# Kernel tuning notes

Measured on AMD Instinct MI355X. Metric: run time of the kernel, lower is better.

Reference implementation:

```python
import jax, jax.numpy as jnp
import numpy as np

N = 1048576   # samples
C = 64        # classes (Y unique targets)
S = 8         # subgroups


def setup_inputs() -> dict:
    key = jax.random.key(0)
    k1, k2, k3 = jax.random.split(key, 3)
    logits = jax.random.normal(k1, (N, C), dtype=jnp.float32)
    targets = jax.random.randint(k2, (N,), 0, C, dtype=jnp.int64)
    subgroup_inf = jax.random.randint(k3, (N,), 0, S, dtype=jnp.int64)
    return {"logits": logits, "targets": targets, "subgroup_inf": subgroup_inf}


def reference(logits, targets, subgroup_inf):
    # per-sample cross-entropy (loss_fn with reduction='none')
    logp = jax.nn.log_softmax(logits, axis=-1)                       # [N, C]
    per_sample = -jnp.take_along_axis(logp, targets[:, None], axis=-1)[:, 0]  # [N]

    # composite (target, subgroup) key -> group counts via one scatter-add
    key_ids = targets * S + subgroup_inf                              # [N]
    counts = jax.ops.segment_sum(jnp.ones_like(per_sample), key_ids,
                                 num_segments=C * S)                  # [C*S]
    # every sample's own group has count >= 1, so no div-by-zero
    weighted = per_sample / counts[key_ids]
    return jnp.sum(weighted)
```

## Files before the change

kernel.cpp:

```cpp
#include <hip/hip_runtime.h>


#define NKEYS 512
#define NSLICES 512
#define ABLOCK 512
typedef float v4f __attribute__((ext_vector_type(4)));

__device__ __forceinline__ float pick4(v4f v, int j) {
    float r = v.x;
    r = (j == 1) ? v.y : r;
    r = (j == 2) ? v.z : r;
    r = (j == 3) ? v.w : r;
    return r;
}

__device__ __forceinline__ float esum4(v4f v) {
    return __expf(v.x) + __expf(v.y) + __expf(v.z) + __expf(v.w);
}

__global__ __launch_bounds__(ABLOCK, 4)
void orl_hist_kernel(const float* __restrict__ logits,
                     const int* __restrict__ targets,
                     const int* __restrict__ subg,
                     float* __restrict__ psum,
                     unsigned int* __restrict__ pcnt,
                     int n) {
    __shared__ float        lsum[NKEYS];
    __shared__ unsigned int lcnt[NKEYS];
    for (int i = threadIdx.x; i < NKEYS; i += ABLOCK) { lsum[i] = 0.0f; lcnt[i] = 0u; }
    __syncthreads();

    const int lane = threadIdx.x & 63;
    const int q    = lane & 15;
    const int g    = lane >> 4;
    const int wave = (blockIdx.x << 3) | (threadIdx.x >> 6);
    const int nwaves = gridDim.x << 3;

    int base = wave * 16;
    for (; base + 16 <= n; base += nwaves * 16) {
        const int r0 = base + g * 4;
        const int4 t4 = *(const int4*)(targets + r0);
        const int4 u4 = *(const int4*)(subg + r0);
        const float* rowp = logits + (size_t)r0 * 64 + q * 4;
        const v4f v0 = __builtin_nontemporal_load((const v4f*)(rowp));
        const v4f v1 = __builtin_nontemporal_load((const v4f*)(rowp + 64));
        const v4f v2 = __builtin_nontemporal_load((const v4f*)(rowp + 128));
        const v4f v3 = __builtin_nontemporal_load((const v4f*)(rowp + 192));

        float s0 = esum4(v0), s1 = esum4(v1), s2 = esum4(v2), s3 = esum4(v3);
        #pragma unroll
        for (int m = 1; m < 16; m <<= 1) {
            s0 += __shfl_xor(s0, m, 16);
            s1 += __shfl_xor(s1, m, 16);
            s2 += __shfl_xor(s2, m, 16);
            s3 += __shfl_xor(s3, m, 16);
        }
        if ((t4.x >> 2) == q) {
            const float ps = __logf(s0) - pick4(v0, t4.x & 3);
            atomicAdd(&lsum[t4.x * 8 + u4.x], ps); atomicAdd(&lcnt[t4.x * 8 + u4.x], 1u);
        }
        if ((t4.y >> 2) == q) {
            const float ps = __logf(s1) - pick4(v1, t4.y & 3);
            atomicAdd(&lsum[t4.y * 8 + u4.y], ps); atomicAdd(&lcnt[t4.y * 8 + u4.y], 1u);
        }
        if ((t4.z >> 2) == q) {
            const float ps = __logf(s2) - pick4(v2, t4.z & 3);
            atomicAdd(&lsum[t4.z * 8 + u4.z], ps); atomicAdd(&lcnt[t4.z * 8 + u4.z], 1u);
        }
        if ((t4.w >> 2) == q) {
            const float ps = __logf(s3) - pick4(v3, t4.w & 3);
            atomicAdd(&lsum[t4.w * 8 + u4.w], ps); atomicAdd(&lcnt[t4.w * 8 + u4.w], 1u);
        }
    }
    for (int o = 0; o < 4; ++o) {
        const int r = base + g * 4 + o;
        if (r < n) {
            const v4f v = *((const v4f*)(logits + (size_t)r * 64) + q);
            const int t = targets[r];
            float s = esum4(v);
            #pragma unroll
            for (int m = 1; m < 16; m <<= 1) s += __shfl_xor(s, m, 16);
            if ((t >> 2) == q) {
                const float ps = __logf(s) - pick4(v, t & 3);
                const int key = t * 8 + subg[r];
                atomicAdd(&lsum[key], ps); atomicAdd(&lcnt[key], 1u);
            }
        }
    }

    __syncthreads();
    const size_t sbase = (size_t)blockIdx.x * NKEYS;
    for (int i = threadIdx.x; i < NKEYS; i += ABLOCK) {
        psum[sbase + i] = lsum[i];
        pcnt[sbase + i] = lcnt[i];
    }
}

__global__ __launch_bounds__(256)
void orl_reduce_kernel(const float* __restrict__ psum,
                       const unsigned int* __restrict__ pcnt,
                       float* __restrict__ out) {
    const int kk  = threadIdx.x & 7;
    const int sl  = threadIdx.x >> 3;
    const int key = (blockIdx.x << 3) | kk;
    float s = 0.0f; unsigned int c = 0u;
    #pragma unroll 4
    for (int b = sl; b < NSLICES; b += 32) {
        s += psum[(size_t)b * NKEYS + key];
        c += pcnt[(size_t)b * NKEYS + key];
    }
    #pragma unroll
    for (int m = 8; m < 64; m <<= 1) {
        s += __shfl_xor(s, m, 64);
        c += __shfl_xor(c, m, 64);
    }
    __shared__ float        ls[4][8];
    __shared__ unsigned int lc[4][8];
    const int w = threadIdx.x >> 6;
    if ((threadIdx.x & 63) < 8) { ls[w][kk] = s; lc[w][kk] = c; }
    __syncthreads();
    if (threadIdx.x < 8) {
        const float        S = ls[0][kk] + ls[1][kk] + ls[2][kk] + ls[3][kk];
        const unsigned int C = lc[0][kk] + lc[1][kk] + lc[2][kk] + lc[3][kk];
        float v = C ? S / (float)C : 0.0f;
        #pragma unroll
        for (int m = 1; m < 8; m <<= 1) v += __shfl_xor(v, m, 8);
        if (threadIdx.x == 0) atomicAdd(out, v);
    }
}

extern "C" void kernel_launch(void* const* d_in, const int* in_sizes, int n_in,
                              void* d_out, int out_size, void* d_ws, size_t ws_size,
                              hipStream_t stream) {
    const float* logits  = (const float*)d_in[0];
    const int*   targets = (const int*)d_in[1];
    const int*   subg    = (const int*)d_in[2];
    const int n = in_sizes[1];
    float* out = (float*)d_out;

    float*        psum = (float*)d_ws;
    unsigned int* pcnt = (unsigned int*)((char*)d_ws + (size_t)NSLICES * NKEYS * 4);

    hipMemsetAsync(out, 0, sizeof(float), stream);
    orl_hist_kernel<<<NSLICES, ABLOCK, 0, stream>>>(logits, targets, subg, psum, pcnt, n);
    orl_reduce_kernel<<<64, 256, 0, stream>>>(psum, pcnt, out);
}
```

Baseline: 351.9 us.

## Precompute group counts first, then divide per sample and drop per-key partials

A separate counting kernel now builds the global (target, subgroup) histogram first. The main kernel then divides each per-sample loss by its group count and accumulates one scalar per thread, so the per-key shared-memory atomics and the slice-partial reduction kernel go away. The launch moves to 2048 blocks of 256 threads, and the logits loads become normal rather than nontemporal. The cost is an extra pass over targets and subgroups, an extra memset, and a per-sample division.

Measured after the change: 373.8 us. 1.06x slower.

```diff
diff --git a/kernel.cpp b/kernel.cpp
--- a/kernel.cpp
+++ b/kernel.cpp
@@ -2,8 +2,6 @@
 
 
 #define NKEYS 512
-#define NSLICES 512
-#define ABLOCK 512
 typedef float v4f __attribute__((ext_vector_type(4)));
 
 __device__ __forceinline__ float pick4(v4f v, int j) {
@@ -18,34 +16,64 @@
     return __expf(v.x) + __expf(v.y) + __expf(v.z) + __expf(v.w);
 }
 
-__global__ __launch_bounds__(ABLOCK, 4)
-void orl_hist_kernel(const float* __restrict__ logits,
+__global__ __launch_bounds__(256)
+void orl_count_kernel(const int* __restrict__ targets,
+                      const int* __restrict__ subg,
+                      unsigned int* __restrict__ cnt,
+                      int n) {
+    __shared__ unsigned int lcnt[NKEYS];
+    for (int i = threadIdx.x; i < NKEYS; i += 256) lcnt[i] = 0u;
+    __syncthreads();
+
+    const int tid = blockIdx.x * 256 + threadIdx.x;
+    const int nthreads = gridDim.x * 256;
+    const int n4 = n >> 2;
+    for (int i4 = tid; i4 < n4; i4 += nthreads) {
+        const int4 t4 = ((const int4*)targets)[i4];
+        const int4 u4 = ((const int4*)subg)[i4];
+        atomicAdd(&lcnt[t4.x * 8 + u4.x], 1u);
+        atomicAdd(&lcnt[t4.y * 8 + u4.y], 1u);
+        atomicAdd(&lcnt[t4.z * 8 + u4.z], 1u);
+        atomicAdd(&lcnt[t4.w * 8 + u4.w], 1u);
+    }
+    for (int i = (n4 << 2) + tid; i < n; i += nthreads)
+        atomicAdd(&lcnt[targets[i] * 8 + subg[i]], 1u);
+
+    __syncthreads();
+    for (int i = threadIdx.x; i < NKEYS; i += 256) {
+        const unsigned int c = lcnt[i];
+        if (c) atomicAdd(&cnt[i], c);
+    }
+}
+
+__global__ __launch_bounds__(256, 6)
+void orl_main_kernel(const float* __restrict__ logits,
                      const int* __restrict__ targets,
                      const int* __restrict__ subg,
-                     float* __restrict__ psum,
-                     unsigned int* __restrict__ pcnt,
+                     const unsigned int* __restrict__ cnt,
+                     float* __restrict__ out,
                      int n) {
-    __shared__ float        lsum[NKEYS];
-    __shared__ unsigned int lcnt[NKEYS];
-    for (int i = threadIdx.x; i < NKEYS; i += ABLOCK) { lsum[i] = 0.0f; lcnt[i] = 0u; }
+    __shared__ float lcf[NKEYS];
+    for (int i = threadIdx.x; i < NKEYS; i += 256) lcf[i] = (float)cnt[i];
     __syncthreads();
 
     const int lane = threadIdx.x & 63;
     const int q    = lane & 15;
     const int g    = lane >> 4;
-    const int wave = (blockIdx.x << 3) | (threadIdx.x >> 6);
-    const int nwaves = gridDim.x << 3;
+    const int wave = (blockIdx.x << 2) | (threadIdx.x >> 6);
+    const int nwaves = gridDim.x << 2;
 
+    float acc = 0.0f;
     int base = wave * 16;
     for (; base + 16 <= n; base += nwaves * 16) {
         const int r0 = base + g * 4;
         const int4 t4 = *(const int4*)(targets + r0);
         const int4 u4 = *(const int4*)(subg + r0);
         const float* rowp = logits + (size_t)r0 * 64 + q * 4;
-        const v4f v0 = __builtin_nontemporal_load((const v4f*)(rowp));
-        const v4f v1 = __builtin_nontemporal_load((const v4f*)(rowp + 64));
-        const v4f v2 = __builtin_nontemporal_load((const v4f*)(rowp + 128));
-        const v4f v3 = __builtin_nontemporal_load((const v4f*)(rowp + 192));
+        const v4f v0 = *(const v4f*)(rowp);
+        const v4f v1 = *(const v4f*)(rowp + 64);
+        const v4f v2 = *(const v4f*)(rowp + 128);
+        const v4f v3 = *(const v4f*)(rowp + 192);
 
         float s0 = esum4(v0), s1 = esum4(v1), s2 = esum4(v2), s3 = esum4(v3);
         #pragma unroll
@@ -55,22 +83,14 @@
             s2 += __shfl_xor(s2, m, 16);
             s3 += __shfl_xor(s3, m, 16);
         }
-        if ((t4.x >> 2) == q) {
-            const float ps = __logf(s0) - pick4(v0, t4.x & 3);
-            atomicAdd(&lsum[t4.x * 8 + u4.x], ps); atomicAdd(&lcnt[t4.x * 8 + u4.x], 1u);
-        }
-        if ((t4.y >> 2) == q) {
-            const float ps = __logf(s1) - pick4(v1, t4.y & 3);
-            atomicAdd(&lsum[t4.y * 8 + u4.y], ps); atomicAdd(&lcnt[t4.y * 8 + u4.y], 1u);
-        }
-        if ((t4.z >> 2) == q) {
-            const float ps = __logf(s2) - pick4(v2, t4.z & 3);
-            atomicAdd(&lsum[t4.z * 8 + u4.z], ps); atomicAdd(&lcnt[t4.z * 8 + u4.z], 1u);
-        }
-        if ((t4.w >> 2) == q) {
-            const float ps = __logf(s3) - pick4(v3, t4.w & 3);
-            atomicAdd(&lsum[t4.w * 8 + u4.w], ps); atomicAdd(&lcnt[t4.w * 8 + u4.w], 1u);
-        }
+        if ((t4.x >> 2) == q)
+            acc += (__logf(s0) - pick4(v0, t4.x & 3)) / lcf[t4.x * 8 + u4.x];
+        if ((t4.y >> 2) == q)
+            acc += (__logf(s1) - pick4(v1, t4.y & 3)) / lcf[t4.y * 8 + u4.y];
+        if ((t4.z >> 2) == q)
+            acc += (__logf(s2) - pick4(v2, t4.z & 3)) / lcf[t4.z * 8 + u4.z];
+        if ((t4.w >> 2) == q)
+            acc += (__logf(s3) - pick4(v3, t4.w & 3)) / lcf[t4.w * 8 + u4.w];
     }
     for (int o = 0; o < 4; ++o) {
         const int r = base + g * 4 + o;
@@ -80,53 +100,18 @@
             float s = esum4(v);
             #pragma unroll
             for (int m = 1; m < 16; m <<= 1) s += __shfl_xor(s, m, 16);
-            if ((t >> 2) == q) {
-                const float ps = __logf(s) - pick4(v, t & 3);
-                const int key = t * 8 + subg[r];
-                atomicAdd(&lsum[key], ps); atomicAdd(&lcnt[key], 1u);
-            }
+            if ((t >> 2) == q)
+                acc += (__logf(s) - pick4(v, t & 3)) / lcf[t * 8 + subg[r]];
         }
     }
 
+    #pragma unroll
+    for (int m = 1; m < 64; m <<= 1) acc += __shfl_xor(acc, m, 64);
+    __shared__ float wsum[4];
+    if (lane == 0) wsum[threadIdx.x >> 6] = acc;
     __syncthreads();
-    const size_t sbase = (size_t)blockIdx.x * NKEYS;
-    for (int i = threadIdx.x; i < NKEYS; i += ABLOCK) {
-        psum[sbase + i] = lsum[i];
-        pcnt[sbase + i] = lcnt[i];
-    }
-}
-
-__global__ __launch_bounds__(256)
-void orl_reduce_kernel(const float* __restrict__ psum,
-                       const unsigned int* __restrict__ pcnt,
-                       float* __restrict__ out) {
-    const int kk  = threadIdx.x & 7;
-    const int sl  = threadIdx.x >> 3;
-    const int key = (blockIdx.x << 3) | kk;
-    float s = 0.0f; unsigned int c = 0u;
-    #pragma unroll 4
-    for (int b = sl; b < NSLICES; b += 32) {
-        s += psum[(size_t)b * NKEYS + key];
-        c += pcnt[(size_t)b * NKEYS + key];
-    }
-    #pragma unroll
-    for (int m = 8; m < 64; m <<= 1) {
-        s += __shfl_xor(s, m, 64);
-        c += __shfl_xor(c, m, 64);
-    }
-    __shared__ float        ls[4][8];
-    __shared__ unsigned int lc[4][8];
-    const int w = threadIdx.x >> 6;
-    if ((threadIdx.x & 63) < 8) { ls[w][kk] = s; lc[w][kk] = c; }
-    __syncthreads();
-    if (threadIdx.x < 8) {
-        const float        S = ls[0][kk] + ls[1][kk] + ls[2][kk] + ls[3][kk];
-        const unsigned int C = lc[0][kk] + lc[1][kk] + lc[2][kk] + lc[3][kk];
-        float v = C ? S / (float)C : 0.0f;
-        #pragma unroll
-        for (int m = 1; m < 8; m <<= 1) v += __shfl_xor(v, m, 8);
-        if (threadIdx.x == 0) atomicAdd(out, v);
-    }
+    if (threadIdx.x == 0)
+        atomicAdd(out, wsum[0] + wsum[1] + wsum[2] + wsum[3]);
 }
 
 extern "C" void kernel_launch(void* const* d_in, const int* in_sizes, int n_in,
@@ -138,10 +123,10 @@
     const int n = in_sizes[1];
     float* out = (float*)d_out;
 
-    float*        psum = (float*)d_ws;
-    unsigned int* pcnt = (unsigned int*)((char*)d_ws + (size_t)NSLICES * NKEYS * 4);
+    unsigned int* cnt = (unsigned int*)d_ws;
 
     hipMemsetAsync(out, 0, sizeof(float), stream);
-    orl_hist_kernel<<<NSLICES, ABLOCK, 0, stream>>>(logits, targets, subg, psum, pcnt, n);
-    orl_reduce_kernel<<<64, 256, 0, stream>>>(psum, pcnt, out);
+    hipMemsetAsync(cnt, 0, NKEYS * sizeof(unsigned int), stream);
+    orl_count_kernel<<<256, 256, 0, stream>>>(targets, subg, cnt, n);
+    orl_main_kernel<<<2048, 256, 0, stream>>>(logits, targets, subg, cnt, out, n);
 }
```
